# Optimization experiments

Hardware: AMD Instinct MI355X
Metric: run time of the kernel (lower is better)

The kernel has to match this reference:

```python
import jax, jax.numpy as jnp
import numpy as np

PI = 3.141592653589793
IMG = 256           # img_size (input_resolution)
CONV = 2 * IMG      # conv_size for linear convolution
PITCH = 6.4e-6      # feature_size (m)
WAVELENGTH = 5.2e-7 # green channel, wavelength_list[1]
DISTANCE = 0.2      # distance_list[1] (m)
SCALE_OUT = 0.95    # scale_output


def make_H(n, pitch, wl, z):
    """Angular-spectrum transfer function, unshifted (fft) frequency order."""
    fx = np.fft.fftfreq(n, d=pitch).astype(np.float64)
    FX, FY = np.meshgrid(fx, fx, indexing='xy')
    fz2 = (1.0 / wl) ** 2 - FX ** 2 - FY ** 2
    prop = fz2 > 0
    kz = 2.0 * np.pi * np.sqrt(np.maximum(fz2, 0.0))
    H = np.exp(1j * kz * z) * prop
    return jnp.asarray(H.astype(np.complex64))


def setup_inputs() -> dict:
    key = jax.random.key(0)
    k1, k2, k3 = jax.random.split(key, 3)
    K, D = 512, 256
    z_e_x = jax.random.normal(k1, (16, D, 64, 64), dtype=jnp.float32)
    poh_dec = jax.random.normal(k2, (16, 1, IMG, IMG), dtype=jnp.float32)
    emb = jax.random.uniform(k3, (K, D), dtype=jnp.float32,
                             minval=-1.0 / K, maxval=1.0 / K)
    H = make_H(CONV, PITCH, WAVELENGTH, DISTANCE)
    return {"z_e_x": z_e_x, "poh_dec": poh_dec, "emb": emb, "H": H}


def vq_straight_through(z_e_x, emb):
    # z_e_x: [B, D, h, w] -> BHWC flatten [N, D]
    B, D, h, w = z_e_x.shape
    ze = jnp.transpose(z_e_x, (0, 2, 3, 1)).reshape(-1, D)
    # squared L2 distances to codebook [N, K]
    d2 = (jnp.sum(ze * ze, axis=1, keepdims=True)
          - 2.0 * ze @ emb.T
          + jnp.sum(emb * emb, axis=1))
    idx = jnp.argmin(d2, axis=1)                      # [N]
    zq = jnp.take(emb, idx, axis=0).reshape(B, h, w, D)
    z_q_x = jnp.transpose(zq, (0, 3, 1, 2))           # BCHW (grads -> emb)
    # straight-through: codebook detached, grad flows to z_e_x
    z_q_x_st = z_e_x + jax.lax.stop_gradient(z_q_x - z_e_x)
    return z_q_x_st, z_q_x


def recon_hologram(poh, H):
    # unit-amplitude phase-only field: exp(i*poh)
    field = jax.lax.complex(jnp.cos(poh), jnp.sin(poh))
    pad = (CONV - IMG) // 2
    padded = jnp.pad(field, ((0, 0), (0, 0), (pad, pad), (pad, pad)))  # zero pad
    u = jnp.fft.fft2(jnp.fft.ifftshift(padded, axes=(-2, -1)), norm='ortho')
    u = H * u
    u = jnp.fft.fftshift(jnp.fft.ifft2(u, norm='ortho'), axes=(-2, -1))
    u = u[..., pad:pad + IMG, pad:pad + IMG]          # center crop
    intensity = (jnp.abs(u) ** 2) * SCALE_OUT
    return jnp.sqrt(intensity)


def reference(z_e_x, poh_dec, emb, H):
    z_q_x_st, z_q_x = vq_straight_through(z_e_x, emb)
    # decoder (external VQGAN blocks) stands in as poh_dec; then Hardtanh(-pi, pi)
    poh = jnp.clip(poh_dec, -PI, PI)
    recon_img = recon_hologram(poh, H)
    return (poh, recon_img, z_e_x, z_q_x)
```

## Files before the change

kernel.cpp:

```cpp
#include <hip/hip_runtime.h>

#define PI_F 3.14159265358979323846f

typedef __attribute__((ext_vector_type(8))) _Float16 f16x8;
typedef __attribute__((ext_vector_type(4))) _Float16 f16x4;
typedef __attribute__((ext_vector_type(4))) float floatx4;

__device__ __forceinline__ void gload16(const void* src, void* dst) {
    __builtin_amdgcn_global_load_lds(
        (const __attribute__((address_space(1))) unsigned int*)src,
        (__attribute__((address_space(3))) unsigned int*)dst, 16, 0, 0);
}

__global__ void k_make_H(float2* __restrict__ Hs) {
    int g = blockIdx.x * 256 + threadIdx.x;
    int ybr = g >> 9, xbr = g & 511;
    int ky = __brev((unsigned)ybr) >> 23;
    int kx = __brev((unsigned)xbr) >> 23;
    double val = 1.0 / (512.0 * 6.4e-6);
    double fy = (double)((ky < 256) ? ky : ky - 512) * val;
    double fx = (double)((kx < 256) ? kx : kx - 512) * val;
    double iw = 1.0 / 5.2e-7;
    double px = fx * fx, py = fy * fy;
    double fz2 = (iw * iw - px) - py;
    float2 h = make_float2(0.f, 0.f);
    if (fz2 > 0.0) {
        double t = sqrt(fz2) * 0.2;
        double fr = t - floor(t);
        double sv, cv;
        sincospi(2.0 * fr, &sv, &cv);
        const double sc = 1.0 / 262144.0;
        h = make_float2((float)(cv * sc), (float)(sv * sc));
    }
    Hs[g] = h;
}

__global__ void k_prep_emb(const float* __restrict__ emb,
                           _Float16* __restrict__ eh,
                           float* __restrict__ eq) {
    int k = blockIdx.x;
    int t = threadIdx.x;
    float v = emb[k * 256 + t];
    eh[k * 256 + t] = (_Float16)v;
    float s = v * v;
    for (int off = 32; off; off >>= 1) s += __shfl_down(s, off);
    __shared__ float red[4];
    if ((t & 63) == 0) red[t >> 6] = s;
    __syncthreads();
    if (t == 0) eq[k] = red[0] + red[1] + red[2] + red[3];
}

__global__ __launch_bounds__(256, 3) void k_vq(const float* __restrict__ ze,
                                               const _Float16* __restrict__ eh,
                                               const float* __restrict__ eq,
                                               int* __restrict__ idx,
                                               float* __restrict__ zeout) {
    __shared__ _Float16 B[2][4096];
    __shared__ _Float16 Ast[4][32][136];
    int tid = threadIdx.x;
    int lane = tid & 63, wave = tid >> 6;
    int n0 = blockIdx.x * 128 + wave * 32;
    int b = n0 >> 12;
    int s0 = n0 & 4095;
    int m = lane & 15;
    int q = lane >> 4;

    const _Float16* srcp = eh + m * 256 + (wave * 4 + q) * 8;

#define STAGE(kt_, buf_)  do {                                               \
        const _Float16* s_ = srcp + (kt_) * 4096;    \
        _Float16* d_ = &B[buf_][wave * 512];                                 \
        gload16(s_,       d_);                                               \
        gload16(s_ + 128, d_ + 2048);         \
    } while (0)

    STAGE(0, 0);

    const float* zb = ze + (size_t)b * (256 * 4096);
    float* zo = zeout ? zeout + (size_t)b * (256 * 4096) : nullptr;
    int g = lane >> 3;
    int s4 = lane & 7;
    f16x8 a[2][8];
#pragma unroll
    for (int half = 0; half < 2; ++half) {
#pragma unroll
        for (int c2 = 0; c2 < 4; ++c2) {
            int c = half * 4 + c2;
            float vv[4][4];
#pragma unroll
            for (int dd = 0; dd < 4; ++dd) {
                int d = c * 32 + g * 4 + dd;
                size_t off = (size_t)d * 4096 + s0 + s4 * 4;
                float4 t = *(const float4*)&zb[off];
                if (zeout) *(float4*)&zo[off] = t;
                vv[dd][0] = t.x; vv[dd][1] = t.y;
                vv[dd][2] = t.z; vv[dd][3] = t.w;
            }
#pragma unroll
            for (int i = 0; i < 4; ++i) {
                f16x4 p = {(_Float16)vv[0][i], (_Float16)vv[1][i],
                           (_Float16)vv[2][i], (_Float16)vv[3][i]};
                *(f16x4*)&Ast[wave][s4 * 4 + i][c2 * 32 + g * 4] = p;
            }
        }
#pragma unroll
        for (int c2 = 0; c2 < 4; ++c2)
#pragma unroll
            for (int T = 0; T < 2; ++T)
                a[T][half * 4 + c2] =
                    *(const f16x8*)&Ast[wave][T * 16 + m][c2 * 32 + q * 8];
    }
    __syncthreads();

    float best[2][4];
    int bidx[2][4];
#pragma unroll
    for (int T = 0; T < 2; ++T)
#pragma unroll
        for (int r = 0; r < 4; ++r) { best[T][r] = 3.4e38f; bidx[T][r] = 0x7fffffff; }

    int cur = 0;
    for (int kt = 0; kt < 32; ++kt) {
        if (kt < 31) STAGE(kt + 1, cur ^ 1);

        int kc = kt * 16 + m;
        float eqv = eq[kc];
        floatx4 acc0 = {0.f, 0.f, 0.f, 0.f};
        floatx4 acc1 = {0.f, 0.f, 0.f, 0.f};
        const _Float16* b0 = &B[cur][q * 128 + m * 8];
#pragma unroll
        for (int c = 0; c < 8; ++c) {
            f16x8 bb = *(const f16x8*)(b0 + c * 512);
            acc0 = __builtin_amdgcn_mfma_f32_16x16x32_f16(a[0][c], bb, acc0, 0, 0, 0);
            acc1 = __builtin_amdgcn_mfma_f32_16x16x32_f16(a[1][c], bb, acc1, 0, 0, 0);
        }
#pragma unroll
        for (int r = 0; r < 4; ++r) {
            float d0 = eqv - 2.0f * acc0[r];
            if (d0 < best[0][r]) { best[0][r] = d0; bidx[0][r] = kc; }
            float d1 = eqv - 2.0f * acc1[r];
            if (d1 < best[1][r]) { best[1][r] = d1; bidx[1][r] = kc; }
        }
        __syncthreads();
        cur ^= 1;
    }
#undef STAGE

#pragma unroll
    for (int T = 0; T < 2; ++T)
#pragma unroll
        for (int r = 0; r < 4; ++r) {
            float bv = best[T][r];
            int bi = bidx[T][r];
            for (int off = 1; off < 16; off <<= 1) {
                float ov = __shfl_xor(bv, off);
                int oi = __shfl_xor(bi, off);
                if (ov < bv || (ov == bv && oi < bi)) { bv = ov; bi = oi; }
            }
            if (m == 0) idx[n0 + T * 16 + q * 4 + r] = bi;
        }
}

__global__ __launch_bounds__(256) void k_zq(const float* __restrict__ emb,
                                            const int* __restrict__ idx,
                                            float* __restrict__ out4) {
    __shared__ float E[32 * 257];
    __shared__ int sidx[32];
    int tid = threadIdx.x;
    int blk = blockIdx.x;
    int b = blk >> 7;
    int s0 = (blk & 127) << 5;
    if (tid < 32) sidx[tid] = idx[(b << 12) + s0 + tid];
    __syncthreads();
#pragma unroll
    for (int i = 0; i < 32; ++i)
        E[i * 257 + tid] = emb[sidx[i] * 256 + tid];
    __syncthreads();
    float* ob = out4 + ((size_t)b << 20) + s0;
    int s_off = tid & 31, d0 = tid >> 5;
#pragma unroll
    for (int i2 = 0; i2 < 32; ++i2) {
        int d = d0 + (i2 << 3);
        ob[((size_t)d << 12) + s_off] = E[s_off * 257 + d];
    }
}

__global__ void k_ze(const float* __restrict__ ze, float* __restrict__ out3) {
    size_t g = (size_t)blockIdx.x * 256 + threadIdx.x;
    ((float4*)out3)[g] = ((const float4*)ze)[g];
}

__global__ __launch_bounds__(256) void k_fwd_rows(const float* __restrict__ poh_in,
                                                  float* __restrict__ poh_out,
                                                  float2* __restrict__ F) {
    __shared__ float2 Xs[4][512];
    __shared__ float2 tw[256];
    int tid = threadIdx.x;
    {
        float sv, cv;
        sincospif(-(float)tid * (1.0f / 256.0f), &sv, &cv);
        tw[tid] = make_float2(cv, sv);
    }
    __syncthreads();
    int wave = tid >> 6, lane = tid & 63;
    int b = blockIdx.x >> 6;
    int t = ((blockIdx.x & 63) << 2) + wave;
    int jy = (t < 128) ? t : t + 256;
    int ry = (t < 128) ? t + 128 : t - 128;
    float2* X = Xs[wave];

    const float* prow = poh_in + (b << 16) + (ry << 8);
    float* orow = poh_out + (b << 16) + (ry << 8);
#pragma unroll
    for (int c0 = 0; c0 < 256; c0 += 64) {
        int c = c0 + lane;
        float v = prow[c];
        v = fminf(fmaxf(v, -PI_F), PI_F);
        orow[c] = v;
        float sv, cv;
        __sincosf(v, &sv, &cv);
        int jx = (c < 128) ? c + 384 : c - 128;
        X[jx] = make_float2(cv, sv);
    }
#pragma unroll
    for (int p0 = 128; p0 < 384; p0 += 64) X[p0 + lane] = make_float2(0.f, 0.f);

#pragma unroll
    for (int s = 8; s >= 0; --s) {
        int mm = 1 << s;
#pragma unroll
        for (int it = 0; it < 4; ++it) {
            int tt = it * 64 + lane;
            int j = tt & (mm - 1);
            int i0 = ((tt >> s) << (s + 1)) + j;
            float2 a = X[i0], bb = X[i0 + mm];
            float2 w = tw[j << (8 - s)];
            float dx = a.x - bb.x, dy = a.y - bb.y;
            X[i0] = make_float2(a.x + bb.x, a.y + bb.y);
            X[i0 + mm] = make_float2(dx * w.x - dy * w.y, dx * w.y + dy * w.x);
        }
    }
    float2* Frow = F + ((size_t)(b * 512 + jy) << 9);
#pragma unroll
    for (int p0 = 0; p0 < 512; p0 += 64) Frow[p0 + lane] = X[p0 + lane];
}

__global__ __launch_bounds__(256) void k_cols(float2* __restrict__ F,
                                              const float2* __restrict__ Hs) {
    __shared__ float2 X[8 * 514];
    __shared__ float2 tw[256];
    int tid = threadIdx.x;
    {
        float sv, cv;
        sincospif(-(float)tid * (1.0f / 256.0f), &sv, &cv);
        tw[tid] = make_float2(cv, sv);
    }
    int b = blockIdx.x >> 6;
    int jx0 = (blockIdx.x & 63) << 3;
    const size_t ibase = ((size_t)b << 18);

#pragma unroll
    for (int i0 = 0; i0 < 8 * 256; i0 += 256) {
        int ii = i0 + tid;
        int col = ii & 7, rr = ii >> 3;
        int jy = (rr < 128) ? rr : rr + 256;
        X[col * 514 + jy] = F[ibase + ((size_t)jy << 9) + jx0 + col];
    }
#pragma unroll
    for (int i0 = 0; i0 < 8 * 256; i0 += 256) {
        int ii = i0 + tid;
        int col = ii & 7, rr = ii >> 3;
        X[col * 514 + 128 + rr] = make_float2(0.f, 0.f);
    }
    __syncthreads();

    int wave = tid >> 6, lane = tid & 63;
    int colh = lane >> 5;
    int r = lane & 31;
    float2* Xc = X + (wave * 2 + colh) * 514;

#pragma unroll
    for (int s = 8; s >= 0; --s) {
        int mm = 1 << s;
#pragma unroll
        for (int it = 0; it < 8; ++it) {
            int tt = it * 32 + r;
            int j = tt & (mm - 1);
            int i0 = ((tt >> s) << (s + 1)) + j;
            float2 a = Xc[i0], bb = Xc[i0 + mm];
            float2 ww = tw[j << (8 - s)];
            float dx = a.x - bb.x, dy = a.y - bb.y;
            Xc[i0] = make_float2(a.x + bb.x, a.y + bb.y);
            Xc[i0 + mm] = make_float2(dx * ww.x - dy * ww.y, dx * ww.y + dy * ww.x);
        }
    }
    {
        int gc = jx0 + wave * 2 + colh;
#pragma unroll
        for (int p0 = 0; p0 < 512; p0 += 32) {
            int p = p0 + r;
            float2 h = Hs[((size_t)p << 9) + gc];
            float2 v = Xc[p];
            Xc[p] = make_float2(v.x * h.x - v.y * h.y,
                                v.x * h.y + v.y * h.x);
        }
    }
#pragma unroll
    for (int s = 0; s <= 8; ++s) {
        int mm = 1 << s;
#pragma unroll
        for (int it = 0; it < 8; ++it) {
            int tt = it * 32 + r;
            int j = tt & (mm - 1);
            int i0 = ((tt >> s) << (s + 1)) + j;
            float2 a = Xc[i0], bb = Xc[i0 + mm];
            float2 ww = tw[j << (8 - s)];
            float bx = bb.x * ww.x + bb.y * ww.y;
            float by = bb.y * ww.x - bb.x * ww.y;
            Xc[i0] = make_float2(a.x + bx, a.y + by);
            Xc[i0 + mm] = make_float2(a.x - bx, a.y - by);
        }
    }
    __syncthreads();
#pragma unroll
    for (int i0 = 0; i0 < 8 * 256; i0 += 256) {
        int ii = i0 + tid;
        int col = ii & 7, rr = ii >> 3;
        int jy = (rr < 128) ? rr : rr + 256;
        F[ibase + ((size_t)jy << 9) + jx0 + col] = X[col * 514 + jy];
    }
}

__global__ __launch_bounds__(256) void k_inv_rows(const float2* __restrict__ F,
                                                  float* __restrict__ out2) {
    __shared__ float2 Xs[4][512];
    __shared__ float2 tw[256];
    int tid = threadIdx.x;
    {
        float sv, cv;
        sincospif(-(float)tid * (1.0f / 256.0f), &sv, &cv);
        tw[tid] = make_float2(cv, sv);
    }
    __syncthreads();
    int wave = tid >> 6, lane = tid & 63;
    int b = blockIdx.x >> 6;
    int t = ((blockIdx.x & 63) << 2) + wave;
    int jy = (t < 128) ? t : t + 256;
    int r = (t < 128) ? t + 128 : t - 128;
    float2* X = Xs[wave];

    const float2* Frow = F + ((size_t)(b * 512 + jy) << 9);
#pragma unroll
    for (int p0 = 0; p0 < 512; p0 += 64) X[p0 + lane] = Frow[p0 + lane];

#pragma unroll
    for (int s = 0; s <= 8; ++s) {
        int mm = 1 << s;
#pragma unroll
        for (int it = 0; it < 4; ++it) {
            int tt = it * 64 + lane;
            int j = tt & (mm - 1);
            int i0 = ((tt >> s) << (s + 1)) + j;
            float2 a = X[i0], bb = X[i0 + mm];
            float2 ww = tw[j << (8 - s)];
            float bx = bb.x * ww.x + bb.y * ww.y;
            float by = bb.y * ww.x - bb.x * ww.y;
            X[i0] = make_float2(a.x + bx, a.y + by);
            X[i0 + mm] = make_float2(a.x - bx, a.y - by);
        }
    }
    float* orow = out2 + (b << 16) + (r << 8);
    const float SC = 0.97467943448f;
#pragma unroll
    for (int c0 = 0; c0 < 256; c0 += 64) {
        int c = c0 + lane;
        int jx = (c < 128) ? c + 384 : c - 128;
        float2 u = X[jx];
        orow[c] = sqrtf(u.x * u.x + u.y * u.y) * SC;
    }
}

extern "C" void kernel_launch(void* const* d_in, const int* in_sizes, int n_in,
                              void* d_out, int out_size, void* d_ws, size_t ws_size,
                              hipStream_t stream) {
    const float* ze  = (const float*)d_in[0];
    const float* poh = (const float*)d_in[1];
    const float* emb = (const float*)d_in[2];

    float* out  = (float*)d_out;
    float* out1 = out;
    float* out2 = out + 1048576;
    float* out3 = out + 2097152;
    float* out4 = out + 18874368;

    const size_t WS_NEED = 262144 + 2048 + 262144 + 2097152;
    bool fused = (d_ws != nullptr) && (ws_size >= WS_NEED);
    char* base = fused ? (char*)d_ws : (char*)out3;
    _Float16* eh;
    float* eq;
    int* idxp;
    float2* Hs;
    if (fused) {
        eh   = (_Float16*)base;
        eq   = (float*)(base + 262144);
        idxp = (int*)(base + 264192);
        Hs   = (float2*)(base + 526336);
    } else {
        eh   = (_Float16*)base;
        eq   = (float*)(base + 262144);
        idxp = (int*)(base + 264192);
        Hs   = (float2*)(base + 1048576);
    }
    float2* F = (float2*)out4;

    k_make_H  <<<1024, 256, 0, stream>>>(Hs);
    k_prep_emb<<<512, 256, 0, stream>>>(emb, eh, eq);
    k_vq      <<<512, 256, 0, stream>>>(ze, eh, eq, idxp,
                                        fused ? out3 : (float*)nullptr);
    k_fwd_rows<<<1024, 256, 0, stream>>>(poh, out1, F);
    k_cols    <<<1024, 256, 0, stream>>>(F, Hs);
    k_inv_rows<<<1024, 256, 0, stream>>>(F, out2);
    k_zq      <<<2048, 256, 0, stream>>>(emb, idxp, out4);
    if (!fused)
        k_ze  <<<16384, 256, 0, stream>>>(ze, out3);
}
```

Baseline: 299.3 us.

## Use radix-8 register FFT passes with swizzled LDS layout in FFT kernels

Replaces the nine radix-2 LDS butterfly stages in the row, column and inverse-row FFT kernels with three radix-8 passes done in registers, each loading 8 points, doing three butterfly levels, then writing back. This cuts LDS round-trips per element from nine to three. An XOR swizzle on LDS indices is added to reduce bank conflicts from power-of-two strides. It raises register pressure per thread and relies on the swizzle staying consistent across every LDS access.

```diff
diff --git a/kernel.cpp b/kernel.cpp
--- a/kernel.cpp
+++ b/kernel.cpp
@@ -10,6 +10,99 @@
     __builtin_amdgcn_global_load_lds(
         (const __attribute__((address_space(1))) unsigned int*)src,
         (__attribute__((address_space(3))) unsigned int*)dst, 16, 0, 0);
+}
+
+__device__ __forceinline__ int swz(int p) { return p ^ ((p >> 5) & 15); }
+
+__device__ __forceinline__ float2 cadd(float2 a, float2 b) {
+    return make_float2(a.x + b.x, a.y + b.y);
+}
+__device__ __forceinline__ float2 csub(float2 a, float2 b) {
+    return make_float2(a.x - b.x, a.y - b.y);
+}
+__device__ __forceinline__ float2 cmul(float2 a, float2 w) {
+    return make_float2(a.x * w.x - a.y * w.y, a.x * w.y + a.y * w.x);
+}
+__device__ __forceinline__ float2 cmulc(float2 a, float2 w) {
+    return make_float2(a.x * w.x + a.y * w.y, a.y * w.x - a.x * w.y);
+}
+
+template <int S>
+__device__ __forceinline__ void dif_triple(float2* X, const float2* tw, int ss) {
+    const int Q = 1 << (S - 2);
+    int block = ss >> (S - 2);
+    int j0 = ss & (Q - 1);
+    int base = (block << (S + 1)) + j0;
+    float2 v[8];
+#pragma unroll
+    for (int t = 0; t < 8; ++t) v[t] = X[swz(base + t * Q)];
+#pragma unroll
+    for (int t = 0; t < 4; ++t) {
+        float2 w = tw[(j0 + t * Q) << (8 - S)];
+        float2 a = v[t], b = v[t + 4];
+        v[t] = cadd(a, b);
+        v[t + 4] = cmul(csub(a, b), w);
+    }
+#pragma unroll
+    for (int h = 0; h < 2; ++h)
+#pragma unroll
+        for (int t0 = 0; t0 < 2; ++t0) {
+            int t = h * 4 + t0;
+            float2 w = tw[(j0 + t0 * Q) << (9 - S)];
+            float2 a = v[t], b = v[t + 2];
+            v[t] = cadd(a, b);
+            v[t + 2] = cmul(csub(a, b), w);
+        }
+    {
+        float2 w = tw[j0 << (10 - S)];
+#pragma unroll
+        for (int t = 0; t < 8; t += 2) {
+            float2 a = v[t], b = v[t + 1];
+            v[t] = cadd(a, b);
+            v[t + 1] = cmul(csub(a, b), w);
+        }
+    }
+#pragma unroll
+    for (int t = 0; t < 8; ++t) X[swz(base + t * Q)] = v[t];
+}
+
+template <int S>
+__device__ __forceinline__ void dit_triple(float2* X, const float2* tw, int ss) {
+    const int Q = 1 << (S - 2);
+    int block = ss >> (S - 2);
+    int j0 = ss & (Q - 1);
+    int base = (block << (S + 1)) + j0;
+    float2 v[8];
+#pragma unroll
+    for (int t = 0; t < 8; ++t) v[t] = X[swz(base + t * Q)];
+    {
+        float2 w = tw[j0 << (10 - S)];
+#pragma unroll
+        for (int t = 0; t < 8; t += 2) {
+            float2 a = v[t], b = cmulc(v[t + 1], w);
+            v[t] = cadd(a, b);
+            v[t + 1] = csub(a, b);
+        }
+    }
+#pragma unroll
+    for (int h = 0; h < 2; ++h)
+#pragma unroll
+        for (int t0 = 0; t0 < 2; ++t0) {
+            int t = h * 4 + t0;
+            float2 w = tw[(j0 + t0 * Q) << (9 - S)];
+            float2 a = v[t], b = cmulc(v[t + 2], w);
+            v[t] = cadd(a, b);
+            v[t + 2] = csub(a, b);
+        }
+#pragma unroll
+    for (int t = 0; t < 4; ++t) {
+        float2 w = tw[(j0 + t * Q) << (8 - S)];
+        float2 a = v[t], b = cmulc(v[t + 4], w);
+        v[t] = cadd(a, b);
+        v[t + 4] = csub(a, b);
+    }
+#pragma unroll
+    for (int t = 0; t < 8; ++t) X[swz(base + t * Q)] = v[t];
 }
 
 __global__ void k_make_H(float2* __restrict__ Hs) {
@@ -220,29 +313,18 @@
         float sv, cv;
         __sincosf(v, &sv, &cv);
         int jx = (c < 128) ? c + 384 : c - 128;
-        X[jx] = make_float2(cv, sv);
-    }
-#pragma unroll
-    for (int p0 = 128; p0 < 384; p0 += 64) X[p0 + lane] = make_float2(0.f, 0.f);
-
-#pragma unroll
-    for (int s = 8; s >= 0; --s) {
-        int mm = 1 << s;
-#pragma unroll
-        for (int it = 0; it < 4; ++it) {
-            int tt = it * 64 + lane;
-            int j = tt & (mm - 1);
-            int i0 = ((tt >> s) << (s + 1)) + j;
-            float2 a = X[i0], bb = X[i0 + mm];
-            float2 w = tw[j << (8 - s)];
-            float dx = a.x - bb.x, dy = a.y - bb.y;
-            X[i0] = make_float2(a.x + bb.x, a.y + bb.y);
-            X[i0 + mm] = make_float2(dx * w.x - dy * w.y, dx * w.y + dy * w.x);
-        }
-    }
+        X[swz(jx)] = make_float2(cv, sv);
+    }
+#pragma unroll
+    for (int p0 = 128; p0 < 384; p0 += 64) X[swz(p0 + lane)] = make_float2(0.f, 0.f);
+
+    dif_triple<8>(X, tw, lane);
+    dif_triple<5>(X, tw, lane);
+    dif_triple<2>(X, tw, lane);
+
     float2* Frow = F + ((size_t)(b * 512 + jy) << 9);
 #pragma unroll
-    for (int p0 = 0; p0 < 512; p0 += 64) Frow[p0 + lane] = X[p0 + lane];
+    for (int p0 = 0; p0 < 512; p0 += 64) Frow[p0 + lane] = X[swz(p0 + lane)];
 }
 
 __global__ __launch_bounds__(256) void k_cols(float2* __restrict__ F,
@@ -264,13 +346,13 @@
         int ii = i0 + tid;
         int col = ii & 7, rr = ii >> 3;
         int jy = (rr < 128) ? rr : rr + 256;
-        X[col * 514 + jy] = F[ibase + ((size_t)jy << 9) + jx0 + col];
+        X[col * 514 + swz(jy)] = F[ibase + ((size_t)jy << 9) + jx0 + col];
     }
 #pragma unroll
     for (int i0 = 0; i0 < 8 * 256; i0 += 256) {
         int ii = i0 + tid;
         int col = ii & 7, rr = ii >> 3;
-        X[col * 514 + 128 + rr] = make_float2(0.f, 0.f);
+        X[col * 514 + swz(128 + rr)] = make_float2(0.f, 0.f);
     }
     __syncthreads();
 
@@ -279,55 +361,32 @@
     int r = lane & 31;
     float2* Xc = X + (wave * 2 + colh) * 514;
 
-#pragma unroll
-    for (int s = 8; s >= 0; --s) {
-        int mm = 1 << s;
-#pragma unroll
-        for (int it = 0; it < 8; ++it) {
-            int tt = it * 32 + r;
-            int j = tt & (mm - 1);
-            int i0 = ((tt >> s) << (s + 1)) + j;
-            float2 a = Xc[i0], bb = Xc[i0 + mm];
-            float2 ww = tw[j << (8 - s)];
-            float dx = a.x - bb.x, dy = a.y - bb.y;
-            Xc[i0] = make_float2(a.x + bb.x, a.y + bb.y);
-            Xc[i0 + mm] = make_float2(dx * ww.x - dy * ww.y, dx * ww.y + dy * ww.x);
-        }
-    }
+    dif_triple<8>(Xc, tw, r);       dif_triple<8>(Xc, tw, 32 + r);
+    dif_triple<5>(Xc, tw, r);       dif_triple<5>(Xc, tw, 32 + r);
+    dif_triple<2>(Xc, tw, r);       dif_triple<2>(Xc, tw, 32 + r);
+
     {
         int gc = jx0 + wave * 2 + colh;
 #pragma unroll
         for (int p0 = 0; p0 < 512; p0 += 32) {
             int p = p0 + r;
             float2 h = Hs[((size_t)p << 9) + gc];
-            float2 v = Xc[p];
-            Xc[p] = make_float2(v.x * h.x - v.y * h.y,
-                                v.x * h.y + v.y * h.x);
-        }
-    }
-#pragma unroll
-    for (int s = 0; s <= 8; ++s) {
-        int mm = 1 << s;
-#pragma unroll
-        for (int it = 0; it < 8; ++it) {
-            int tt = it * 32 + r;
-            int j = tt & (mm - 1);
-            int i0 = ((tt >> s) << (s + 1)) + j;
-            float2 a = Xc[i0], bb = Xc[i0 + mm];
-            float2 ww = tw[j << (8 - s)];
-            float bx = bb.x * ww.x + bb.y * ww.y;
-            float by = bb.y * ww.x - bb.x * ww.y;
-            Xc[i0] = make_float2(a.x + bx, a.y + by);
-            Xc[i0 + mm] = make_float2(a.x - bx, a.y - by);
-        }
-    }
+            int qs = swz(p);
+            Xc[qs] = cmul(Xc[qs], h);
+        }
+    }
+
+    dit_triple<2>(Xc, tw, r);       dit_triple<2>(Xc, tw, 32 + r);
+    dit_triple<5>(Xc, tw, r);       dit_triple<5>(Xc, tw, 32 + r);
+    dit_triple<8>(Xc, tw, r);       dit_triple<8>(Xc, tw, 32 + r);
+
     __syncthreads();
 #pragma unroll
     for (int i0 = 0; i0 < 8 * 256; i0 += 256) {
         int ii = i0 + tid;
         int col = ii & 7, rr = ii >> 3;
         int jy = (rr < 128) ? rr : rr + 256;
-        F[ibase + ((size_t)jy << 9) + jx0 + col] = X[col * 514 + jy];
+        F[ibase + ((size_t)jy << 9) + jx0 + col] = X[col * 514 + swz(jy)];
     }
 }
 
@@ -351,31 +410,19 @@
 
     const float2* Frow = F + ((size_t)(b * 512 + jy) << 9);
 #pragma unroll
-    for (int p0 = 0; p0 < 512; p0 += 64) X[p0 + lane] = Frow[p0 + lane];
-
-#pragma unroll
-    for (int s = 0; s <= 8; ++s) {
-        int mm = 1 << s;
-#pragma unroll
-        for (int it = 0; it < 4; ++it) {
-            int tt = it * 64 + lane;
-            int j = tt & (mm - 1);
-            int i0 = ((tt >> s) << (s + 1)) + j;
-            float2 a = X[i0], bb = X[i0 + mm];
-            float2 ww = tw[j << (8 - s)];
-            float bx = bb.x * ww.x + bb.y * ww.y;
-            float by = bb.y * ww.x - bb.x * ww.y;
-            X[i0] = make_float2(a.x + bx, a.y + by);
-            X[i0 + mm] = make_float2(a.x - bx, a.y - by);
-        }
-    }
+    for (int p0 = 0; p0 < 512; p0 += 64) X[swz(p0 + lane)] = Frow[p0 + lane];
+
+    dit_triple<2>(X, tw, lane);
+    dit_triple<5>(X, tw, lane);
+    dit_triple<8>(X, tw, lane);
+
     float* orow = out2 + (b << 16) + (r << 8);
     const float SC = 0.97467943448f;
 #pragma unroll
     for (int c0 = 0; c0 < 256; c0 += 64) {
         int c = c0 + lane;
         int jx = (c < 128) ? c + 384 : c - 128;
-        float2 u = X[jx];
+        float2 u = X[swz(jx)];
         orow[c] = sqrtf(u.x * u.x + u.y * u.y) * SC;
     }
 }
```

Result: faster. 277.9 us (-7.2%).
